# Kernel optimization log

Measured on AMD Instinct MI355X. Metric: run time of the kernel, lower is better.

The kernel has to match this reference:

```python
import jax, jax.numpy as jnp
import numpy as np

B, C, H, W = 2, 192, 128, 128
WS, OWS, HEADS = 16, 24, 6           # window, overlap window, heads
PAD = (OWS - WS) // 2
SCALE = (C // HEADS) ** -0.5
EPS = 1e-6


def _calc_rpi(ws, ows):
    co = np.stack(np.meshgrid(np.arange(ws), np.arange(ws), indexing='ij')).reshape(2, -1)
    ce = np.stack(np.meshgrid(np.arange(ows), np.arange(ows), indexing='ij')).reshape(2, -1)
    rel = (ce[:, None, :] - co[:, :, None]).transpose(1, 2, 0).astype(np.int64)  # (ws^2, ows^2, 2)
    rel[..., 0] += ws - ows + 1
    rel[..., 1] += ws - ows + 1
    rel[..., 0] *= ws + ows - 1
    idx = rel.sum(-1)
    # torch indexes the bias table with negative indices (python wraparound) -> explicit mod
    return np.mod(idx, (ws + ows - 1) ** 2)

RPI = jnp.asarray(_calc_rpi(WS, OWS))  # (WS*WS, OWS*OWS)


def _ln2d(x, g, b):  # LayerNorm2d over channel dim of (b,c,h,w)
    mu = jnp.mean(x, axis=1, keepdims=True)
    var = jnp.mean((x - mu) ** 2, axis=1, keepdims=True)
    return (x - mu) / jnp.sqrt(var + EPS) * g[None, :, None, None] + b[None, :, None, None]


def _conv1x1(x, w, b):  # x (b,c,h,w), w (o,c)
    return jnp.einsum('bchw,oc->bohw', x, w) + b[None, :, None, None]


def _window_partition(x, ws):  # (b,h,w,c) -> (b*nw, ws, ws, c)
    b, h, w, c = x.shape
    x = x.reshape(b, h // ws, ws, w // ws, ws, c).transpose(0, 1, 3, 2, 4, 5)
    return x.reshape(-1, ws, ws, c)


def _window_reverse(win, ws, h, w):  # (b*nw, ws, ws, c) -> (b,h,w,c)
    b = win.shape[0] // (h * w // ws // ws)
    x = win.reshape(b, h // ws, w // ws, ws, ws, -1).transpose(0, 1, 3, 2, 4, 5)
    return x.reshape(b, h, w, -1)


def _oca(x, qkv_w, qkv_b, rpb):  # overlapping-window cross attention; x (b,c,h,w), normalized
    b, c, h, w = x.shape
    qkv = jnp.einsum('bhwc,oc->bhwo', x.transpose(0, 2, 3, 1), qkv_w) + qkv_b
    qkv = qkv.reshape(b, h, w, 3, c).transpose(3, 0, 4, 1, 2)  # (3,b,c,h,w)
    q = qkv[0].transpose(0, 2, 3, 1)                            # (b,h,w,c)
    kv = jnp.concatenate([qkv[1], qkv[2]], axis=1)              # (b,2c,h,w)
    qw = _window_partition(q, WS).reshape(-1, WS * WS, c)
    # nn.Unfold(kernel=OWS, stride=WS, padding=PAD) replicated with padded gather
    p = jnp.pad(kv, ((0, 0), (0, 0), (PAD, PAD), (PAD, PAD)))
    nH, nW = h // WS, w // WS
    rows = (jnp.arange(nH) * WS)[:, None] + jnp.arange(OWS)[None, :]  # (nH, OWS)
    cols = (jnp.arange(nW) * WS)[:, None] + jnp.arange(OWS)[None, :]
    p = p[:, :, rows, :]            # (b,2c,nH,OWS,Wp)
    p = p[:, :, :, :, cols]         # (b,2c,nH,OWS,nW,OWS)
    p = p.reshape(b, 2, c, nH, OWS, nW, OWS).transpose(1, 0, 3, 5, 4, 6, 2)
    p = p.reshape(2, b * nH * nW, OWS * OWS, c)
    kwin, vwin = p[0], p[1]
    d = c // HEADS
    b_ = qw.shape[0]
    qh = qw.reshape(b_, WS * WS, HEADS, d).transpose(0, 2, 1, 3) * SCALE
    kh = kwin.reshape(b_, OWS * OWS, HEADS, d).transpose(0, 2, 1, 3)
    vh = vwin.reshape(b_, OWS * OWS, HEADS, d).transpose(0, 2, 1, 3)
    attn = jnp.einsum('bhqd,bhkd->bhqk', qh, kh)
    bias = rpb[RPI.reshape(-1)].reshape(WS * WS, OWS * OWS, HEADS).transpose(2, 0, 1)
    attn = jax.nn.softmax(attn + bias[None], axis=-1)
    out = jnp.einsum('bhqk,bhkd->bhqd', attn, vh).transpose(0, 2, 1, 3).reshape(b_, WS * WS, c)
    return _window_reverse(out.reshape(-1, WS, WS, c), WS, h, w)  # (b,h,w,c)


def setup_inputs() -> dict:
    key = jax.random.key(0)
    ks = jax.random.split(key, 16)
    s = 0.02
    return {
        'x_l': jax.random.normal(ks[0], (B, C, H, W), jnp.float32),
        'x_r': jax.random.normal(ks[1], (B, C, H, W), jnp.float32),
        'qkv_w': jax.random.normal(ks[2], (3 * C, C), jnp.float32) * s,
        'qkv_b': jnp.zeros((3 * C,), jnp.float32),
        'rpb_table': jax.random.normal(ks[3], ((WS + OWS - 1) ** 2, HEADS), jnp.float32) * s,
        'norm_l_g': jnp.ones((C,), jnp.float32),
        'norm_l_b': jnp.zeros((C,), jnp.float32),
        'norm_r_g': jnp.ones((C,), jnp.float32),
        'norm_r_b': jnp.zeros((C,), jnp.float32),
        'lp1_w': jax.random.normal(ks[4], (C, C), jnp.float32) * s,
        'lp1_b': jnp.zeros((C,), jnp.float32),
        'rp1_w': jax.random.normal(ks[5], (C, C), jnp.float32) * s,
        'rp1_b': jnp.zeros((C,), jnp.float32),
        'lp2_w': jax.random.normal(ks[6], (C, C), jnp.float32) * s,
        'lp2_b': jnp.zeros((C,), jnp.float32),
        'rp2_w': jax.random.normal(ks[7], (C, C), jnp.float32) * s,
        'rp2_b': jnp.zeros((C,), jnp.float32),
        'beta': jax.random.normal(ks[8], (1, C, 1, 1), jnp.float32) * s,
        'gamma': jax.random.normal(ks[9], (1, C, 1, 1), jnp.float32) * s,
    }


def reference(x_l, x_r, qkv_w, qkv_b, rpb_table, norm_l_g, norm_l_b, norm_r_g, norm_r_b,
              lp1_w, lp1_b, rp1_w, rp1_b, lp2_w, lp2_b, rp2_w, rp2_b, beta, gamma):
    nl = _ln2d(x_l, norm_l_g, norm_l_b)   # torch overwrites x_l with norm_l(x_l)
    nr = _ln2d(x_r, norm_r_g, norm_r_b)
    xl_ = _oca(nl, qkv_w, qkv_b, rpb_table)   # (b,h,w,c)
    xr_ = _oca(nr, qkv_w, qkv_b, rpb_table)
    Q_l = _conv1x1(_ln2d(xl_.transpose(0, 3, 2, 1), norm_l_g, norm_l_b), lp1_w, lp1_b).transpose(0, 2, 3, 1)  # (b,w,h,c)
    Q_r_T = _conv1x1(_ln2d(xr_.transpose(0, 3, 2, 1), norm_r_g, norm_r_b), rp1_w, rp1_b).transpose(0, 2, 1, 3)  # (b,w,c,h)
    V_l = _conv1x1(nl, lp2_w, lp2_b).transpose(0, 2, 3, 1)
    V_r = _conv1x1(nr, rp2_w, rp2_b).transpose(0, 2, 3, 1)
    att = jnp.matmul(Q_l, Q_r_T) * SCALE                       # (b,w,h,h) epipolar attention
    F_r2l = jnp.matmul(jax.nn.softmax(att, axis=-1), V_r)
    F_l2r = jnp.matmul(jax.nn.softmax(att.transpose(0, 1, 3, 2), axis=-1), V_l)
    out_l = nl + F_r2l.transpose(0, 3, 1, 2) * beta
    out_r = nr + F_l2r.transpose(0, 3, 1, 2) * gamma
    return (out_l, out_r)
```

## Files before the change

### kernel.cpp

```cpp
#include <hip/hip_runtime.h>
#include <stdint.h>

typedef short bf16x8 __attribute__((ext_vector_type(8)));
typedef float f32x4 __attribute__((ext_vector_type(4)));

__device__ inline float bf2f(uint16_t u){ uint32_t v = ((uint32_t)u)<<16; float f; __builtin_memcpy(&f,&v,4); return f; }
__device__ inline float ubf(uint32_t u){ float f; __builtin_memcpy(&f,&u,4); return f; }
__device__ inline uint16_t f2bf(float f){ uint32_t u; __builtin_memcpy(&u,&f,4); u += 0x7fffu + ((u>>16)&1u); return (uint16_t)(u>>16); }
__device__ inline uint16_t f2bfr(float f){ uint32_t u; __builtin_memcpy(&u,&f,4); return (uint16_t)((u + 0x8000u)>>16); }

#define CCH   192
#define HH    128
#define WWD   128
#define HWSZ  16384
#define NPOS_SIDE 32768
#define NPOS  65536
#define NKT   576
#define SCALE_F 0.17677669529663687f
#define SCALE2_F 0.2550348727f

__global__ __launch_bounds__(256) void k_cvtw(const float* qkvw, const float* l1, const float* r1,
        const float* l2, const float* r2,
        uint16_t* wq, uint16_t* w1l, uint16_t* w1r, uint16_t* w2l, uint16_t* w2r){
    int which = blockIdx.y;
    int i = blockIdx.x*256 + threadIdx.x;
    const float* src; uint16_t* dst; int n;
    switch(which){
      case 0: src=qkvw; dst=wq;  n=576*192; break;
      case 1: src=l1;   dst=w1l; n=192*192; break;
      case 2: src=r1;   dst=w1r; n=192*192; break;
      case 3: src=l2;   dst=w2l; n=192*192; break;
      default:src=r2;   dst=w2r; n=192*192; break;
    }
    if(i<n) dst[i] = f2bf(src[i]);
}

__global__ __launch_bounds__(256) void k_bias(const float* rpb, uint2* biasQ){
    int e = blockIdx.x*256 + threadIdx.x;
    if(e >= 6*256*18*8) return;
    int k = e & 7;
    int c = (e >> 3) % 18;
    int q = ((e >> 3) / 18) % 256;
    int h = e / (8*18*256);
    int half = k >> 2, lg = k & 3;
    int qi = q >> 4, qj = q & 15;
    uint32_t w0 = 0, w1 = 0;
    #pragma unroll
    for(int r=0;r<4;r++){
        int kt = c*32 + half*16 + lg*4 + r;
        int ki = kt/24, kj = kt%24;
        int id = (ki - qi - 7)*39 + (kj - qj - 7);
        id %= 1521; if(id < 0) id += 1521;
        uint32_t bv = f2bf(rpb[id*6 + h] * 1.4426950408889634f);
        if(r < 2) w0 |= bv << (16*r); else w1 |= bv << (16*(r-2));
    }
    biasQ[e] = make_uint2(w0, w1);
}

__global__ __launch_bounds__(256) void k_ln1(const float* xl, const float* xr,
        const float* gl, const float* bl, const float* gr, const float* br,
        uint16_t* nlr_bf){
    int pos = blockIdx.x*256 + threadIdx.x;
    int s   = pos >> 15;
    int loc = pos & 32767;
    const float* x = s ? xr : xl;
    const float* g = s ? gr : gl;
    const float* b = s ? br : bl;
    int bb = loc >> 14, hw = loc & 16383;
    const float* xp = x + (size_t)bb*CCH*HWSZ + hw;
    float sum=0.f, sq=0.f;
    for(int c=0;c<CCH;c++){ float v = xp[(size_t)c*HWSZ]; sum+=v; sq+=v*v; }
    float mean = sum*(1.f/192.f);
    float var  = sq*(1.f/192.f) - mean*mean;
    float rstd = rsqrtf(var + 1e-6f);
    uint16_t* obp = nlr_bf + (size_t)pos*CCH;
    for(int cb=0; cb<24; cb++){
        alignas(16) uint16_t tmp[8];
        #pragma unroll
        for(int k=0;k<8;k++){
            int c = cb*8+k;
            float y = (xp[(size_t)c*HWSZ]-mean)*rstd*g[c] + b[c];
            tmp[k] = f2bf(y);
        }
        *(uint4*)(obp + cb*8) = *(const uint4*)tmp;
    }
}

__global__ __launch_bounds__(256) void k_gemm4(const uint16_t* __restrict__ x2,
        const uint16_t* __restrict__ nlr_bf,
        const uint16_t* __restrict__ w1l, const uint16_t* __restrict__ w1r,
        const uint16_t* __restrict__ w2l, const uint16_t* __restrict__ w2r,
        const float* __restrict__ lp1b, const float* __restrict__ rp1b,
        const float* __restrict__ lp2b, const float* __restrict__ rp2b,
        uint16_t* __restrict__ QLb, uint16_t* __restrict__ QRb,
        uint16_t* __restrict__ VLb, uint16_t* __restrict__ VRb){
    const int K = 192, N = 192;
    int z = blockIdx.z;
    const uint16_t* A; const uint16_t* W; const float* bias; uint16_t* out;
    switch(z){
      case 0: A = x2;                          W = w1l; bias = lp1b; out = QLb; break;
      case 1: A = x2 + (size_t)32768*192;      W = w1r; bias = rp1b; out = QRb; break;
      case 2: A = nlr_bf;                      W = w2l; bias = lp2b; out = VLb; break;
      default:A = nlr_bf + (size_t)32768*192;  W = w2r; bias = rp2b; out = VRb; break;
    }
    int tid = threadIdx.x;
    int w = tid >> 6, lane = tid & 63;
    int lr = lane & 15, lg = lane >> 4;
    int row0 = blockIdx.y*128 + w*16;
    int col0 = blockIdx.x*64;
    const uint16_t* Ap0 = A + (size_t)(row0 + lr)*K + lg*8;
    const uint16_t* Ap1 = Ap0 + (size_t)64*K;
    const uint16_t* Wp = W + (size_t)col0*K + lg*8;
    f32x4 acc[2][4] = {};
    for(int kk=0; kk<6; kk++){
        bf16x8 a0 = *(const bf16x8*)(Ap0 + kk*32);
        bf16x8 a1 = *(const bf16x8*)(Ap1 + kk*32);
        #pragma unroll
        for(int nf=0; nf<4; nf++){
            bf16x8 bfr = *(const bf16x8*)(Wp + (size_t)(nf*16 + lr)*K + kk*32);
            acc[0][nf] = __builtin_amdgcn_mfma_f32_16x16x32_bf16(a0, bfr, acc[0][nf], 0,0,0);
            acc[1][nf] = __builtin_amdgcn_mfma_f32_16x16x32_bf16(a1, bfr, acc[1][nf], 0,0,0);
        }
    }
    #pragma unroll
    for(int nf=0; nf<4; nf++){
        int col = col0 + nf*16 + lr;
        float bv = bias[col];
        #pragma unroll
        for(int m=0; m<2; m++){
            #pragma unroll
            for(int r=0;r<4;r++){
                int row = row0 + m*64 + lg*4 + r;
                out[(size_t)row*N + col] = f2bf(acc[m][nf][r] + bv);
            }
        }
    }
}

__global__ __launch_bounds__(256) void k_gemmw(const uint16_t* __restrict__ A,
        const uint16_t* __restrict__ W, const float* __restrict__ bias,
        uint16_t* __restrict__ out, int K, int N){
    int tid = threadIdx.x;
    int w = tid >> 6, lane = tid & 63;
    int lr = lane & 15, lg = lane >> 4;
    int row0 = blockIdx.y*128 + w*16;
    int col0 = blockIdx.x*192;
    const uint16_t* Ap0 = A + (size_t)(row0 + lr)*K + lg*8;
    const uint16_t* Ap1 = Ap0 + (size_t)64*K;
    const uint16_t* Wp = W + (size_t)col0*K + lg*8;
    f32x4 acc[2][12] = {};
    int ksteps = K >> 5;
    for(int kk=0; kk<ksteps; kk++){
        bf16x8 a0 = *(const bf16x8*)(Ap0 + kk*32);
        bf16x8 a1 = *(const bf16x8*)(Ap1 + kk*32);
        #pragma unroll
        for(int nf=0; nf<12; nf++){
            bf16x8 bfr = *(const bf16x8*)(Wp + (size_t)(nf*16 + lr)*K + kk*32);
            acc[0][nf] = __builtin_amdgcn_mfma_f32_16x16x32_bf16(a0, bfr, acc[0][nf], 0,0,0);
            acc[1][nf] = __builtin_amdgcn_mfma_f32_16x16x32_bf16(a1, bfr, acc[1][nf], 0,0,0);
        }
    }
    #pragma unroll
    for(int nf=0; nf<12; nf++){
        int col = col0 + nf*16 + lr;
        float bv = bias[col];
        #pragma unroll
        for(int m=0; m<2; m++){
            #pragma unroll
            for(int r=0;r<4;r++){
                int row = row0 + m*64 + lg*4 + r;
                out[(size_t)row*N + col] = f2bf(acc[m][nf][r] + bv);
            }
        }
    }
}

#define KPAD 40
#define STG  192
#define VTP  200
__global__ __launch_bounds__(256) void k_attn(const uint16_t* __restrict__ qkv,
        const uint2* __restrict__ biasQ, uint16_t* __restrict__ attout){
    __shared__ uint16_t Ks[STG*KPAD];
    __shared__ uint16_t Vt[32*VTP];

    int bid = blockIdx.x;
    int s = bid / 768; int r1 = bid % 768;
    int b = r1 / 384;  int r2 = r1 % 384;
    int head = r2 / 64; int win = r2 % 64;
    int hb = win >> 3, wb = win & 7;
    int tid = threadIdx.x;
    int posbase = s*NPOS_SIDE + b*HWSZ;

    int wv = tid >> 6, lane = tid & 63;
    int lr = lane & 15, lg = lane >> 4;

    bf16x8 qB[4];
    #pragma unroll
    for(int f=0; f<4; f++){
        int t = wv*64 + f*16 + lr;
        int pos = posbase + (hb*16 + (t>>4))*WWD + (wb*16 + (t&15));
        qB[f] = *(const bf16x8*)(qkv + (size_t)pos*NKT + head*32 + lg*8);
    }

    f32x4 acc[4][2] = {};
    float psum[4] = {0.f, 0.f, 0.f, 0.f};

    const uint16_t* kvbase = qkv + (size_t)posbase*NKT;
    const uint2* biasH = biasQ + (size_t)head*256*18*8;

    for(int stg=0; stg<3; stg++){
        __syncthreads();
        for(int idx = tid; idx < STG*4; idx += 256){
            int ktl = idx >> 2, part = idx & 3;
            int ktg = stg*STG + ktl;
            int i = ktg/24, j = ktg%24;
            int h = hb*16 + i - 4, wv2 = wb*16 + j - 4;
            uint4 kd = {0,0,0,0}, vd = {0,0,0,0};
            if((unsigned)h < 128u && (unsigned)wv2 < 128u){
                const uint16_t* p = kvbase + (size_t)(h*WWD + wv2)*NKT + 192 + head*32 + part*8;
                kd = *(const uint4*)p;
                vd = *(const uint4*)(p + 192);
            }
            *(uint4*)(Ks + ktl*KPAD + part*8) = kd;
            int t32 = ktl & 31;
            int ktp = (ktl & ~31) + (((t32&12)<<1) + ((t32>>4)<<2) + (t32&3));
            const uint16_t* vs = (const uint16_t*)&vd;
            #pragma unroll
            for(int k2=0;k2<8;k2++) Vt[(part*8+k2)*VTP + ktp] = vs[k2];
        }
        __syncthreads();

        for(int kc=0; kc<6; kc++){
            int kt0 = kc*32;
            int cg  = stg*6 + kc;
            bf16x8 k0 = *(const bf16x8*)(Ks + (kt0 + lr)*KPAD + lg*8);
            bf16x8 k1 = *(const bf16x8*)(Ks + (kt0 + 16 + lr)*KPAD + lg*8);
            bf16x8 vb0 = *(const bf16x8*)(Vt + lr*VTP        + kt0 + lg*8);
            bf16x8 vb1 = *(const bf16x8*)(Vt + (16+lr)*VTP   + kt0 + lg*8);

            #pragma unroll
            for(int f=0; f<4; f++){
                f32x4 z = {0.f,0.f,0.f,0.f};
                f32x4 s0 = __builtin_amdgcn_mfma_f32_16x16x32_bf16(k0, qB[f], z, 0,0,0);
                f32x4 s1 = __builtin_amdgcn_mfma_f32_16x16x32_bf16(k1, qB[f], z, 0,0,0);
                int q = wv*64 + f*16 + lr;
                const uint2* bq = biasH + ((size_t)q*18 + cg)*8;
                uint2 bh0 = bq[lg];
                uint2 bh1 = bq[4 + lg];
                float e0 = exp2f(__builtin_fmaf(s0[0], SCALE2_F, ubf(bh0.x << 16)));
                float e1 = exp2f(__builtin_fmaf(s0[1], SCALE2_F, ubf(bh0.x & 0xffff0000u)));
                float e2 = exp2f(__builtin_fmaf(s0[2], SCALE2_F, ubf(bh0.y << 16)));
                float e3 = exp2f(__builtin_fmaf(s0[3], SCALE2_F, ubf(bh0.y & 0xffff0000u)));
                float e4 = exp2f(__builtin_fmaf(s1[0], SCALE2_F, ubf(bh1.x << 16)));
                float e5 = exp2f(__builtin_fmaf(s1[1], SCALE2_F, ubf(bh1.x & 0xffff0000u)));
                float e6 = exp2f(__builtin_fmaf(s1[2], SCALE2_F, ubf(bh1.y << 16)));
                float e7 = exp2f(__builtin_fmaf(s1[3], SCALE2_F, ubf(bh1.y & 0xffff0000u)));
                psum[f] += ((e0+e1)+(e2+e3)) + ((e4+e5)+(e6+e7));
                bf16x8 pv;
                pv[0] = (short)f2bfr(e0); pv[1] = (short)f2bfr(e1);
                pv[2] = (short)f2bfr(e2); pv[3] = (short)f2bfr(e3);
                pv[4] = (short)f2bfr(e4); pv[5] = (short)f2bfr(e5);
                pv[6] = (short)f2bfr(e6); pv[7] = (short)f2bfr(e7);
                acc[f][0] = __builtin_amdgcn_mfma_f32_16x16x32_bf16(pv, vb0, acc[f][0], 0,0,0);
                acc[f][1] = __builtin_amdgcn_mfma_f32_16x16x32_bf16(pv, vb1, acc[f][1], 0,0,0);
            }
        }
    }

    #pragma unroll
    for(int f=0; f<4; f++){
        float dsum = psum[f];
        dsum += __shfl_xor(dsum, 16);
        dsum += __shfl_xor(dsum, 32);
        float invl = 1.f / dsum;
        #pragma unroll
        for(int r=0;r<4;r++){
            float inv = __shfl(invl, 4*lg + r);
            int q = wv*64 + f*16 + 4*lg + r;
            int pos = posbase + (hb*16 + (q>>4))*WWD + (wb*16 + (q&15));
            #pragma unroll
            for(int n=0;n<2;n++){
                attout[(size_t)pos*CCH + head*32 + n*16 + lr] = f2bf(acc[f][n][r]*inv);
            }
        }
    }
}

__global__ __launch_bounds__(256) void k_ln2(const uint16_t* __restrict__ attout,
        const float* gl, const float* bl, const float* gr, const float* br,
        uint16_t* __restrict__ x2){
    int wv = threadIdx.x >> 6, lane = threadIdx.x & 63;
    int pos = blockIdx.x*4 + wv;
    int s = pos >> 15;
    const float* g = s ? gr : gl;
    const float* b = s ? br : bl;
    const uint16_t* ip = attout + (size_t)pos*CCH;
    float v[3]; float sum=0.f, sq=0.f;
    #pragma unroll
    for(int k=0;k<3;k++){ v[k] = bf2f(ip[lane + 64*k]); sum += v[k]; sq += v[k]*v[k]; }
    #pragma unroll
    for(int m=1;m<64;m<<=1){ sum += __shfl_xor(sum,m); sq += __shfl_xor(sq,m); }
    float mean = sum*(1.f/192.f);
    float var  = sq*(1.f/192.f) - mean*mean;
    float rstd = rsqrtf(var + 1e-6f);
    uint16_t* op = x2 + (size_t)pos*CCH;
    #pragma unroll
    for(int k=0;k<3;k++){
        int c = lane + 64*k;
        op[c] = f2bf((v[k]-mean)*rstd*g[c] + b[c]);
    }
}

__global__ __launch_bounds__(512) void k_cross1(const uint16_t* __restrict__ QL,
        const uint16_t* __restrict__ QR, uint16_t* __restrict__ Prow, uint16_t* __restrict__ PcolT){
    __shared__ float S[128*128];
    __shared__ float cred[4][128];
    __shared__ float colm[128];
    __shared__ float colinv[128];
    int bid = blockIdx.x; int b = bid >> 7, x = bid & 127;
    int tid = threadIdx.x;
    int wv = tid>>6, lane = tid&63, lr = lane&15, lg = lane>>4;
    const uint16_t* Abase = QL + (size_t)b*HWSZ*CCH;
    const uint16_t* Bbase = QR + (size_t)b*HWSZ*CCH;
    f32x4 acc[8] = {};
    for(int kk=0; kk<6; kk++){
        int i = wv*16 + lr;
        bf16x8 af = *(const bf16x8*)(Abase + (size_t)(i*WWD + x)*CCH + kk*32 + lg*8);
        #pragma unroll
        for(int nf=0; nf<8; nf++){
            int j = nf*16 + lr;
            bf16x8 bfr = *(const bf16x8*)(Bbase + (size_t)(j*WWD + x)*CCH + kk*32 + lg*8);
            acc[nf] = __builtin_amdgcn_mfma_f32_16x16x32_bf16(af, bfr, acc[nf], 0,0,0);
        }
    }
    #pragma unroll
    for(int nf=0;nf<8;nf++)
    #pragma unroll
    for(int r=0;r<4;r++){
        int i = wv*16 + lg*4 + r; int j = nf*16 + lr;
        S[i*128 + j] = acc[nf][r]*SCALE_F;
    }
    __syncthreads();
    uint16_t* prb = Prow + (size_t)(b*128 + x)*128*128;
    for(int i = wv*16; i < wv*16+16; i++){
        float v0 = S[i*128 + lane], v1 = S[i*128 + 64 + lane];
        float m = fmaxf(v0,v1);
        #pragma unroll
        for(int k=1;k<64;k<<=1) m = fmaxf(m, __shfl_xor(m,k));
        float e0 = __expf(v0-m), e1 = __expf(v1-m);
        float ss = e0+e1;
        #pragma unroll
        for(int k=1;k<64;k<<=1) ss += __shfl_xor(ss,k);
        float inv = 1.f/ss;
        prb[i*128 + lane]      = f2bf(e0*inv);
        prb[i*128 + 64 + lane] = f2bf(e1*inv);
    }
    int j = tid & 127, q4 = tid >> 7;
    int i0 = q4*32;
    float m = -1e30f;
    for(int i=i0; i<i0+32; i++) m = fmaxf(m, S[i*128 + j]);
    cred[q4][j] = m;
    __syncthreads();
    if(tid < 128) colm[tid] = fmaxf(fmaxf(cred[0][tid], cred[1][tid]), fmaxf(cred[2][tid], cred[3][tid]));
    __syncthreads();
    float mj = colm[j];
    float ssum = 0.f;
    for(int i=i0; i<i0+32; i++) ssum += __expf(S[i*128 + j] - mj);
    cred[q4][j] = ssum;
    __syncthreads();
    if(tid < 128) colinv[tid] = 1.f/(cred[0][tid] + cred[1][tid] + cred[2][tid] + cred[3][tid]);
    __syncthreads();
    float cinv = colinv[j];
    uint16_t* pcb = PcolT + (size_t)(b*128 + x)*128*128;
    for(int i=i0; i<i0+32; i++) pcb[j*128 + i] = f2bf(__expf(S[i*128 + j] - mj)*cinv);
}

__global__ __launch_bounds__(512) void k_cross2(const uint16_t* __restrict__ Prow,
        const uint16_t* __restrict__ PcolT, const uint16_t* __restrict__ VR,
        const uint16_t* __restrict__ VL, const uint16_t* __restrict__ nlr_bf,
        const float* __restrict__ beta, const float* __restrict__ gamma, float* __restrict__ out){
    __shared__ uint16_t VT[192*136];
    int bid = blockIdx.x; int b = bid>>7, x = bid&127;
    int tid = threadIdx.x;
    int wv = tid>>6, lane = tid&63, lr = lane&15, lg = lane>>4;
    const uint16_t* vrs = VR + (size_t)(b*HWSZ + x*WWD)*CCH;
    const uint16_t* vls = VL + (size_t)(b*HWSZ + x*WWD)*CCH;
    const uint16_t* pr = Prow  + (size_t)(b*128+x)*128*128;
    const uint16_t* pc = PcolT + (size_t)(b*128+x)*128*128;

    for(int idx = tid; idx < 128*24; idx += 512){
        int j = idx / 24, cb = idx % 24;
        uint4 d = *(const uint4*)(vrs + j*CCH + cb*8);
        const uint16_t* dd = (const uint16_t*)&d;
        #pragma unroll
        for(int k=0;k<8;k++) VT[(cb*8+k)*136 + j] = dd[k];
    }
    __syncthreads();
    {
        f32x4 acc[12] = {};
        for(int kk=0; kk<4; kk++){
            int i = wv*16 + lr;
            bf16x8 af = *(const bf16x8*)(pr + i*128 + kk*32 + lg*8);
            #pragma unroll
            for(int nf=0; nf<12; nf++){
                bf16x8 bfr = *(const bf16x8*)(VT + (nf*16+lr)*136 + kk*32 + lg*8);
                acc[nf] = __builtin_amdgcn_mfma_f32_16x16x32_bf16(af, bfr, acc[nf], 0,0,0);
            }
        }
        #pragma unroll
        for(int nf=0; nf<12; nf++){
            int c = nf*16 + lr;
            float bv = beta[c];
            int i0 = wv*16 + lg*4;
            size_t o = ((size_t)(b*CCH + c)*128 + x)*128 + i0;
            const uint16_t* nb = nlr_bf + ((size_t)(b*HWSZ + x*WWD + i0))*CCH + c;
            float4 ov;
            ov.x = bf2f(nb[0*CCH]) + acc[nf][0]*bv;
            ov.y = bf2f(nb[1*CCH]) + acc[nf][1]*bv;
            ov.z = bf2f(nb[2*CCH]) + acc[nf][2]*bv;
            ov.w = bf2f(nb[3*CCH]) + acc[nf][3]*bv;
            *(float4*)(out + o) = ov;
        }
    }
    __syncthreads();
    for(int idx = tid; idx < 128*24; idx += 512){
        int j = idx / 24, cb = idx % 24;
        uint4 d = *(const uint4*)(vls + j*CCH + cb*8);
        const uint16_t* dd = (const uint16_t*)&d;
        #pragma unroll
        for(int k=0;k<8;k++) VT[(cb*8+k)*136 + j] = dd[k];
    }
    __syncthreads();
    {
        f32x4 acc[12] = {};
        for(int kk=0; kk<4; kk++){
            int j = wv*16 + lr;
            bf16x8 af = *(const bf16x8*)(pc + j*128 + kk*32 + lg*8);
            #pragma unroll
            for(int nf=0; nf<12; nf++){
                bf16x8 bfr = *(const bf16x8*)(VT + (nf*16+lr)*136 + kk*32 + lg*8);
                acc[nf] = __builtin_amdgcn_mfma_f32_16x16x32_bf16(af, bfr, acc[nf], 0,0,0);
            }
        }
        float* outr = out + 6291456;
        #pragma unroll
        for(int nf=0; nf<12; nf++){
            int c = nf*16 + lr;
            float gv = gamma[c];
            int j0 = wv*16 + lg*4;
            size_t o = ((size_t)(b*CCH + c)*128 + x)*128 + j0;
            const uint16_t* nb = nlr_bf + ((size_t)(NPOS_SIDE + b*HWSZ + x*WWD + j0))*CCH + c;
            float4 ov;
            ov.x = bf2f(nb[0*CCH]) + acc[nf][0]*gv;
            ov.y = bf2f(nb[1*CCH]) + acc[nf][1]*gv;
            ov.z = bf2f(nb[2*CCH]) + acc[nf][2]*gv;
            ov.w = bf2f(nb[3*CCH]) + acc[nf][3]*gv;
            *(float4*)(outr + o) = ov;
        }
    }
}

extern "C" void kernel_launch(void* const* d_in, const int* in_sizes, int n_in,
                              void* d_out, int out_size, void* d_ws, size_t ws_size,
                              hipStream_t stream){
    const float* x_l   = (const float*)d_in[0];
    const float* x_r   = (const float*)d_in[1];
    const float* qkv_w = (const float*)d_in[2];
    const float* qkv_b = (const float*)d_in[3];
    const float* rpb   = (const float*)d_in[4];
    const float* gl    = (const float*)d_in[5];
    const float* bl    = (const float*)d_in[6];
    const float* gr    = (const float*)d_in[7];
    const float* br    = (const float*)d_in[8];
    const float* lp1w  = (const float*)d_in[9];
    const float* lp1b  = (const float*)d_in[10];
    const float* rp1w  = (const float*)d_in[11];
    const float* rp1b  = (const float*)d_in[12];
    const float* lp2w  = (const float*)d_in[13];
    const float* lp2b  = (const float*)d_in[14];
    const float* rp2w  = (const float*)d_in[15];
    const float* rp2b  = (const float*)d_in[16];
    const float* beta  = (const float*)d_in[17];
    const float* gamma = (const float*)d_in[18];
    float* out = (float*)d_out;

    char* ws = (char*)d_ws;
    uint16_t* nlr_bf  = (uint16_t*)(ws + 0);
    uint16_t* qkv_bf  = (uint16_t*)(ws + 25165824);
    uint16_t* x2      = (uint16_t*)(ws + 25165824);
    uint16_t* QLb     = (uint16_t*)(ws + 50331648);
    uint16_t* QRb     = (uint16_t*)(ws + 62914560);
    uint16_t* Prow    = (uint16_t*)(ws + 75497472);
    uint16_t* PcolT   = (uint16_t*)(ws + 83886080);
    uint2*    bias_q  = (uint2*)   (ws + 100663296);
    uint16_t* attout  = (uint16_t*)(ws + 102432768);
    uint16_t* VLb     = (uint16_t*)(ws + 102432768);
    uint16_t* VRb     = (uint16_t*)(ws + 115015680);
    uint16_t* wq      = (uint16_t*)(ws + 127598592);
    uint16_t* w1l     = (uint16_t*)(ws + 127819776);
    uint16_t* w1r     = (uint16_t*)(ws + 127893504);
    uint16_t* w2l     = (uint16_t*)(ws + 127967232);
    uint16_t* w2r     = (uint16_t*)(ws + 128040960);

    k_cvtw<<<dim3(432,5), 256, 0, stream>>>(qkv_w, lp1w, rp1w, lp2w, rp2w, wq, w1l, w1r, w2l, w2r);
    k_bias<<<864, 256, 0, stream>>>(rpb, bias_q);
    k_ln1<<<256, 256, 0, stream>>>(x_l, x_r, gl, bl, gr, br, nlr_bf);
    k_gemmw<<<dim3(3, 512), 256, 0, stream>>>(nlr_bf, wq, qkv_b, qkv_bf, 192, 576);
    k_attn<<<1536, 256, 0, stream>>>(qkv_bf, bias_q, attout);
    k_ln2<<<16384, 256, 0, stream>>>(attout, gl, bl, gr, br, x2);
    k_gemm4<<<dim3(3, 256, 4), 256, 0, stream>>>(x2, nlr_bf, w1l, w1r, w2l, w2r,
                                                 lp1b, rp1b, lp2b, rp2b, QLb, QRb, VLb, VRb);
    k_cross1<<<256, 512, 0, stream>>>(QLb, QRb, Prow, PcolT);
    k_cross2<<<256, 512, 0, stream>>>(Prow, PcolT, VRb, VLb, nlr_bf, beta, gamma, out);
}
```

Baseline: 354.9 us.

## Relayout attention bias table for coalesced loads and tile LayerNorm through LDS

The relative-position bias table is reordered so each lane group of the attention kernel reads consecutive uint2 entries (indexed by lr fastest), instead of strided per-query rows, which makes the bias loads coalesced. The first LayerNorm now stages a 64-position by 192-channel tile in shared memory, splits the reduction across four waves, and writes bf16 output with four threads per position. It runs with more blocks (1024) than before, giving more parallelism and coalesced writes, at the cost of extra syncs and LDS usage.

```diff
diff --git a/kernel.cpp b/kernel.cpp
--- a/kernel.cpp
+++ b/kernel.cpp
@@ -37,12 +37,15 @@
 
 __global__ __launch_bounds__(256) void k_bias(const float* rpb, uint2* biasQ){
     int e = blockIdx.x*256 + threadIdx.x;
-    if(e >= 6*256*18*8) return;
-    int k = e & 7;
-    int c = (e >> 3) % 18;
-    int q = ((e >> 3) / 18) % 256;
-    int h = e / (8*18*256);
-    int half = k >> 2, lg = k & 3;
+    if(e >= 6*18*16*2*4*16) return;
+    int lr   = e & 15;
+    int lg   = (e >> 4) & 3;
+    int half = (e >> 6) & 1;
+    int qb   = (e >> 7) & 15;
+    int hc   = e >> 11;
+    int c    = hc % 18;
+    int h    = hc / 18;
+    int q = qb*16 + lr;
     int qi = q >> 4, qj = q & 15;
     uint32_t w0 = 0, w1 = 0;
     #pragma unroll
@@ -57,32 +60,63 @@
     biasQ[e] = make_uint2(w0, w1);
 }
 
+#define LNP 65
 __global__ __launch_bounds__(256) void k_ln1(const float* xl, const float* xr,
         const float* gl, const float* bl, const float* gr, const float* br,
         uint16_t* nlr_bf){
-    int pos = blockIdx.x*256 + threadIdx.x;
-    int s   = pos >> 15;
-    int loc = pos & 32767;
+    __shared__ float L[192*LNP];
+    __shared__ float redA[4][64];
+    __shared__ float redB[4][64];
+    __shared__ float mrs[2][64];
+    int pos0 = blockIdx.x * 64;
+    int s   = pos0 >> 15;
+    int loc = pos0 & 32767;
     const float* x = s ? xr : xl;
     const float* g = s ? gr : gl;
     const float* b = s ? br : bl;
-    int bb = loc >> 14, hw = loc & 16383;
-    const float* xp = x + (size_t)bb*CCH*HWSZ + hw;
-    float sum=0.f, sq=0.f;
-    for(int c=0;c<CCH;c++){ float v = xp[(size_t)c*HWSZ]; sum+=v; sq+=v*v; }
-    float mean = sum*(1.f/192.f);
-    float var  = sq*(1.f/192.f) - mean*mean;
-    float rstd = rsqrtf(var + 1e-6f);
-    uint16_t* obp = nlr_bf + (size_t)pos*CCH;
-    for(int cb=0; cb<24; cb++){
-        alignas(16) uint16_t tmp[8];
-        #pragma unroll
-        for(int k=0;k<8;k++){
-            int c = cb*8+k;
-            float y = (xp[(size_t)c*HWSZ]-mean)*rstd*g[c] + b[c];
-            tmp[k] = f2bf(y);
-        }
-        *(uint4*)(obp + cb*8) = *(const uint4*)tmp;
+    int bb = loc >> 14, hw0 = loc & 16383;
+    const float* xp = x + (size_t)bb*CCH*HWSZ + hw0;
+    int tid = threadIdx.x;
+    {
+        int p = tid & 63, cq = tid >> 6;
+        for(int c = cq; c < 192; c += 4)
+            L[c*LNP + p] = xp[(size_t)c*HWSZ + p];
+    }
+    __syncthreads();
+    {
+        int p = tid & 63, part = tid >> 6;
+        float sum = 0.f, sq = 0.f;
+        for(int c = part*48; c < part*48+48; c++){
+            float v = L[c*LNP + p];
+            sum += v; sq += v*v;
+        }
+        redA[part][p] = sum; redB[part][p] = sq;
+    }
+    __syncthreads();
+    if(tid < 64){
+        int p = tid;
+        float sum = redA[0][p]+redA[1][p]+redA[2][p]+redA[3][p];
+        float sq  = redB[0][p]+redB[1][p]+redB[2][p]+redB[3][p];
+        float mean = sum*(1.f/192.f);
+        float var  = sq*(1.f/192.f) - mean*mean;
+        mrs[0][p] = mean;
+        mrs[1][p] = rsqrtf(var + 1e-6f);
+    }
+    __syncthreads();
+    {
+        int p = tid >> 2, tp = tid & 3;
+        float mean = mrs[0][p], rstd = mrs[1][p];
+        uint16_t* obp = nlr_bf + (size_t)(pos0 + p)*CCH + tp*48;
+        for(int cb = 0; cb < 6; cb++){
+            alignas(16) uint16_t tmp[8];
+            #pragma unroll
+            for(int k=0;k<8;k++){
+                int c = tp*48 + cb*8 + k;
+                float y = (L[c*LNP + p]-mean)*rstd*g[c] + b[c];
+                tmp[k] = f2bf(y);
+            }
+            *(uint4*)(obp + cb*8) = *(const uint4*)tmp;
+        }
     }
 }
 
@@ -206,7 +240,7 @@
     float psum[4] = {0.f, 0.f, 0.f, 0.f};
 
     const uint16_t* kvbase = qkv + (size_t)posbase*NKT;
-    const uint2* biasH = biasQ + (size_t)head*256*18*8;
+    const uint2* biasH = biasQ + (size_t)head*36864;
 
     for(int stg=0; stg<3; stg++){
         __syncthreads();
@@ -243,10 +277,10 @@
                 f32x4 z = {0.f,0.f,0.f,0.f};
                 f32x4 s0 = __builtin_amdgcn_mfma_f32_16x16x32_bf16(k0, qB[f], z, 0,0,0);
                 f32x4 s1 = __builtin_amdgcn_mfma_f32_16x16x32_bf16(k1, qB[f], z, 0,0,0);
-                int q = wv*64 + f*16 + lr;
-                const uint2* bq = biasH + ((size_t)q*18 + cg)*8;
-                uint2 bh0 = bq[lg];
-                uint2 bh1 = bq[4 + lg];
+                int qb = wv*4 + f;
+                const uint2* bq = biasH + ((size_t)cg*16 + qb)*128;
+                uint2 bh0 = bq[lg*16 + lr];
+                uint2 bh1 = bq[64 + lg*16 + lr];
                 float e0 = exp2f(__builtin_fmaf(s0[0], SCALE2_F, ubf(bh0.x << 16)));
                 float e1 = exp2f(__builtin_fmaf(s0[1], SCALE2_F, ubf(bh0.x & 0xffff0000u)));
                 float e2 = exp2f(__builtin_fmaf(s0[2], SCALE2_F, ubf(bh0.y << 16)));
@@ -504,7 +538,7 @@
 
     k_cvtw<<<dim3(432,5), 256, 0, stream>>>(qkv_w, lp1w, rp1w, lp2w, rp2w, wq, w1l, w1r, w2l, w2r);
     k_bias<<<864, 256, 0, stream>>>(rpb, bias_q);
-    k_ln1<<<256, 256, 0, stream>>>(x_l, x_r, gl, bl, gr, br, nlr_bf);
+    k_ln1<<<1024, 256, 0, stream>>>(x_l, x_r, gl, bl, gr, br, nlr_bf);
     k_gemmw<<<dim3(3, 512), 256, 0, stream>>>(nlr_bf, wq, qkv_b, qkv_bf, 192, 576);
     k_attn<<<1536, 256, 0, stream>>>(qkv_bf, bias_q, attout);
     k_ln2<<<16384, 256, 0, stream>>>(attout, gl, bl, gr, br, x2);
```

Result: slower. 457.2 us (+28.8%).
